# Kernel tuning notes

Measured on AMD Instinct MI355X. Metric: run time of the kernel, lower is better.

The kernel has to match this reference:

```python
import jax, jax.numpy as jnp
import numpy as np

B, T_OUT, C, L = 8, 8, 64, 1024  # batch, temporal channels, spatial channels (=in_channels), time steps


def setup_inputs() -> dict:
    key = jax.random.key(0)
    ks = jax.random.split(key, 7)
    s = 1.0 / np.sqrt(C)  # conv1d default init scale
    return {
        "x": jax.random.normal(ks[0], (B, T_OUT, C, L), dtype=jnp.float32),
        "Wq": jax.random.uniform(ks[1], (C, C), jnp.float32, -s, s),
        "bq": jax.random.uniform(ks[2], (C,), jnp.float32, -s, s),
        "Wk": jax.random.uniform(ks[3], (C, C), jnp.float32, -s, s),
        "bk": jax.random.uniform(ks[4], (C,), jnp.float32, -s, s),
        "Wv": jax.random.uniform(ks[5], (C, C), jnp.float32, -s, s),
        "bv": jax.random.uniform(ks[6], (C,), jnp.float32, -s, s),
    }


def reference(x, Wq, bq, Wk, bk, Wv, bv):
    b, t, c, l = x.shape
    xr = x.reshape(b * t, c, l)  # [BT, C, L]
    # 1x1 Conv1d == per-timestep linear over channels
    q = jnp.einsum('oc,bcl->bol', Wq, xr) + bq[:, None]
    k = jnp.einsum('oc,bcl->bol', Wk, xr) + bk[:, None]
    v = jnp.einsum('oc,bcl->bol', Wv, xr) + bv[:, None]
    # scores[b, i, j] = sum_c q[b, c, i] * k[b, c, j]  -> [BT, L, L]
    scores = jnp.einsum('bci,bcj->bij', q, k)
    weights = jax.nn.softmax(scores, axis=-1)
    # out[b, i, c] = sum_j weights[b, i, j] * v[b, c, j]
    out = jnp.einsum('bij,bcj->bic', weights, v)
    out = jnp.transpose(out, (0, 2, 1))  # [BT, C, L]
    return out.reshape(b, t, c, l)
```

## Files before the change

### kernel.cpp

```cpp
#include <hip/hip_runtime.h>

#define CC 64
#define LL 1024
#define LOG2E 1.44269504f

typedef unsigned short u16;
typedef unsigned int u32;
typedef __attribute__((ext_vector_type(8))) short short8;
typedef __attribute__((ext_vector_type(4))) float floatx4;

static __device__ __forceinline__ u16 f2b(float f) {
  return (u16)((__float_as_uint(f) + 0x8000u) >> 16);
}
static __device__ __forceinline__ u32 pk2(float a, float b) {
  return ((__float_as_uint(a) + 0x8000u) >> 16) |
         ((__float_as_uint(b) + 0x8000u) & 0xffff0000u);
}
static __device__ __forceinline__ u32 pk2t(float a, float b) {
  return __builtin_amdgcn_perm(__float_as_uint(b), __float_as_uint(a), 0x07060302u);
}
static __device__ __forceinline__ short8 mk8(u32 a, u32 b, u32 c, u32 d) {
  union { u32 u[4]; short8 s; } t;
  t.u[0] = a; t.u[1] = b; t.u[2] = c; t.u[3] = d;
  return t.s;
}

#define LDS_U16 28032

__global__ __launch_bounds__(256) void qkv_kernel(
    const float* __restrict__ x,
    const float* __restrict__ Wq, const float* __restrict__ bq,
    const float* __restrict__ Wk, const float* __restrict__ bk,
    const float* __restrict__ Wv, const float* __restrict__ bv,
    u16* __restrict__ qT, u16* __restrict__ kT, u16* __restrict__ vO)
{
  __shared__ __align__(16) u16 smem_u[LDS_U16];
  u16* const whi_s  = smem_u;
  u16* const xh_s   = smem_u + 13824;
  u16* const tbuf_s = smem_u + 23040;
  float* const b_s  = (float*)(smem_u + 27648);

  const int tid  = threadIdx.x;
  const int wave = tid >> 6;
  const int lane = tid & 63;
  const int l16  = lane & 15;
  const int quad = lane >> 4;

  const int bt = blockIdx.x & 63;
  const int l0 = (blockIdx.x >> 6) << 7;

  const int lx = tid & 63;
  const int cg = (tid >> 6) << 4;
  const float* xp = x + ((size_t)bt * CC + cg) * LL + l0 + lx;

  float v0[16];
  #pragma unroll
  for (int e = 0; e < 16; ++e) v0[e] = xp[(size_t)e * LL];

  #pragma unroll
  for (int rep = 0; rep < 24; ++rep) {
    const int i = (rep * 256 + tid) * 2;
    const int m = i >> 12;
    const int r = (i >> 6) & 63;
    const int c = i & 63;
    const int j = i & 4095;
    const float* W = (m == 0) ? Wq : (m == 1) ? Wk : Wv;
    const float sc = (m == 0) ? LOG2E : 1.0f;
    *(u32*)(whi_s + m * 4608 + r * 72 + c) = pk2(W[j] * sc, W[j + 1] * sc);
  }
  if (tid < 192)
    b_s[tid] = (tid < 64) ? bq[tid] * LOG2E
             : (tid < 128) ? bk[tid - 64] : bv[tid - 128];

  #pragma unroll
  for (int e = 0; e < 16; e += 2)
    *(u32*)(xh_s + lx * 72 + cg + e) = pk2(v0[e], v0[e + 1]);
  __syncthreads();

  float v1[16];
  #pragma unroll
  for (int e = 0; e < 16; ++e) v1[e] = xp[64 + (size_t)e * LL];

  u16* tb = tbuf_s + wave * 1152;

  auto compute = [&](int ch) {
    const int lc0 = l0 + (ch << 6);
    const u16* xr_h = xh_s + ch * 4608 + (wave * 16 + l16) * 72 + quad * 8;
    const short8 xh0 = *(const short8*)(xr_h);
    const short8 xh1 = *(const short8*)(xr_h + 32);

    #pragma unroll
    for (int ot = 0; ot < 12; ++ot) {
      const int m = ot >> 2;
      const int off = m * 4608 + ((ot & 3) * 16 + l16) * 72 + quad * 8;
      const short8 ah0 = *(const short8*)(whi_s + off);
      const short8 ah1 = *(const short8*)(whi_s + off + 32);

      floatx4 acc = (floatx4){0.f, 0.f, 0.f, 0.f};
      acc = __builtin_amdgcn_mfma_f32_16x16x32_bf16(ah0, xh0, acc, 0, 0, 0);
      acc = __builtin_amdgcn_mfma_f32_16x16x32_bf16(ah1, xh1, acc, 0, 0, 0);

      float ov[4];
      #pragma unroll
      for (int r = 0; r < 4; ++r)
        ov[r] = acc[r] + b_s[ot * 16 + quad * 4 + r];

      if (ot < 8) {
        uint2 pv;
        pv.x = pk2(ov[0], ov[1]);
        pv.y = pk2(ov[2], ov[3]);
        *(uint2*)(tb + l16 * 72 + (ot & 3) * 16 + quad * 4) = pv;
        if ((ot & 3) == 3) {
          asm volatile("" ::: "memory");
          u16* gdst = ((ot < 4) ? qT : kT) + ((size_t)(bt * LL + lc0 + wave * 16)) * CC;
          const int rr = lane >> 3;
          const int c8 = (lane & 7) * 8;
          #pragma unroll
          for (int s2 = 0; s2 < 2; ++s2) {
            const int row = s2 * 8 + rr;
            uint4 val = *(const uint4*)(tb + row * 72 + c8);
            *(uint4*)(gdst + row * CC + c8) = val;
          }
          asm volatile("" ::: "memory");
        }
      } else {
        const int ob = (ot - 8) * 16 + quad * 4;
        u16* vdst = vO + ((size_t)(bt * CC + ob)) * LL + lc0 + wave * 16 + l16;
        #pragma unroll
        for (int r = 0; r < 4; ++r)
          vdst[(size_t)r * LL] = f2b(ov[r]);
      }
    }
  };

  compute(0);

  #pragma unroll
  for (int e = 0; e < 16; e += 2)
    *(u32*)(xh_s + 4608 + lx * 72 + cg + e) = pk2(v1[e], v1[e + 1]);
  __syncthreads();

  compute(1);
}

__global__ __launch_bounds__(256) void attn_kernel(
    const u16* __restrict__ qT, const u16* __restrict__ kT,
    const u16* __restrict__ vB, float* __restrict__ out)
{
  __shared__ __align__(16) u16 smem[18432];
  const int tid  = threadIdx.x;
  const int wave = tid >> 6;
  const int lane = tid & 63;
  const int l16  = lane & 15;
  const int quad = lane >> 4;

  const int bt    = blockIdx.x & 63;
  const int chunk = blockIdx.x >> 6;
  const int i0w   = (chunk << 6) + (wave << 4);

  const u16* kbase = kT + (size_t)bt * LL * CC;
  const u16* vbase = vB + (size_t)bt * CC * LL;

  short8 qf[2];
  {
    const u16* qr = qT + (size_t)bt * LL * CC + (size_t)(i0w + l16) * CC + quad * 8;
    qf[0] = *(const short8*)(qr);
    qf[1] = *(const short8*)(qr + 32);
  }

  floatx4 O[4];
  #pragma unroll
  for (int cf = 0; cf < 4; ++cf)
    O[cf] = (floatx4){0.f, 0.f, 0.f, 0.f};
  float lsA = 0.f, lsB = 0.f;

  const int r_st = tid >> 2;
  const int c_st = (tid & 3) << 4;
  const int sr = (r_st & 0x20) | ((r_st & 4) << 2) | ((r_st & 0x18) >> 1) | (r_st & 3);

  {
    uint4 k0 = *(const uint4*)(kbase + (size_t)r_st * CC + c_st);
    uint4 k1 = *(const uint4*)(kbase + (size_t)r_st * CC + c_st + 8);
    uint4 v0 = *(const uint4*)(vbase + (size_t)r_st * LL + c_st);
    uint4 v1 = *(const uint4*)(vbase + (size_t)r_st * LL + c_st + 8);
    *(uint4*)(smem + sr * 72 + c_st)              = k0;
    *(uint4*)(smem + sr * 72 + c_st + 8)          = k1;
    *(uint4*)(smem + 4608 + r_st * 72 + c_st)     = v0;
    *(uint4*)(smem + 4608 + r_st * 72 + c_st + 8) = v1;
  }
  __syncthreads();

  for (int it = 0; it < 16; ++it) {
    u16* ktc = smem + (it & 1) * 9216;
    u16* vtc = ktc + 4608;

    uint4 rk0, rk1, rv0, rv1;
    if (it < 15) {
      const int jb = (it + 1) << 6;
      rk0 = *(const uint4*)(kbase + (size_t)(jb + r_st) * CC + c_st);
      rk1 = *(const uint4*)(kbase + (size_t)(jb + r_st) * CC + c_st + 8);
      rv0 = *(const uint4*)(vbase + (size_t)r_st * LL + jb + c_st);
      rv1 = *(const uint4*)(vbase + (size_t)r_st * LL + jb + c_st + 8);
    }

    floatx4 S[4];
    __builtin_amdgcn_s_setprio(1);
    #pragma unroll
    for (int jt = 0; jt < 4; ++jt) {
      const u16* ka = ktc + (jt * 16 + l16) * 72 + quad * 8;
      const short8 a0 = *(const short8*)(ka);
      const short8 a1 = *(const short8*)(ka + 32);
      floatx4 acc = (floatx4){0.f, 0.f, 0.f, 0.f};
      acc = __builtin_amdgcn_mfma_f32_16x16x32_bf16(a0, qf[0], acc, 0, 0, 0);
      acc = __builtin_amdgcn_mfma_f32_16x16x32_bf16(a1, qf[1], acc, 0, 0, 0);
      S[jt] = acc;
    }
    __builtin_amdgcn_s_setprio(0);

    short8 v0f[4], v1f[4];
    #pragma unroll
    for (int cf = 0; cf < 4; ++cf) {
      const u16* va = vtc + (cf * 16 + l16) * 72 + quad * 8;
      v0f[cf] = *(const short8*)(va);
      v1f[cf] = *(const short8*)(va + 32);
    }

    uint2 pp[4];
    #pragma unroll
    for (int jt = 0; jt < 4; ++jt) {
      const float e0 = __builtin_amdgcn_exp2f(S[jt][0]);
      const float e1 = __builtin_amdgcn_exp2f(S[jt][1]);
      const float e2 = __builtin_amdgcn_exp2f(S[jt][2]);
      const float e3 = __builtin_amdgcn_exp2f(S[jt][3]);
      lsA += e0 + e1;
      lsB += e2 + e3;
      pp[jt].x = pk2t(e0, e1);
      pp[jt].y = pk2t(e2, e3);
    }

    __builtin_amdgcn_s_setprio(1);
    {
      const short8 pa0 = mk8(pp[0].x, pp[0].y, pp[1].x, pp[1].y);
      const short8 pa1 = mk8(pp[2].x, pp[2].y, pp[3].x, pp[3].y);
      #pragma unroll
      for (int cf = 0; cf < 4; ++cf) {
        O[cf] = __builtin_amdgcn_mfma_f32_16x16x32_bf16(pa0, v0f[cf], O[cf], 0, 0, 0);
        O[cf] = __builtin_amdgcn_mfma_f32_16x16x32_bf16(pa1, v1f[cf], O[cf], 0, 0, 0);
      }
    }
    __builtin_amdgcn_s_setprio(0);

    if (it < 15) {
      u16* ktn = smem + ((it + 1) & 1) * 9216;
      *(uint4*)(ktn + sr * 72 + c_st)              = rk0;
      *(uint4*)(ktn + sr * 72 + c_st + 8)          = rk1;
      *(uint4*)(ktn + 4608 + r_st * 72 + c_st)     = rv0;
      *(uint4*)(ktn + 4608 + r_st * 72 + c_st + 8) = rv1;
    }
    __syncthreads();
  }

  float lsum = lsA + lsB;
  lsum += __shfl_xor(lsum, 16, 64);
  lsum += __shfl_xor(lsum, 32, 64);

  __syncthreads();
  float* of = (float*)smem + wave * 1280;
  #pragma unroll
  for (int r = 0; r < 4; ++r) {
    const float rl = __builtin_amdgcn_rcpf(__shfl(lsum, quad * 4 + r, 64));
    #pragma unroll
    for (int cf = 0; cf < 4; ++cf)
      O[cf][r] *= rl;
  }
  asm volatile("" ::: "memory");
  #pragma unroll
  for (int cf = 0; cf < 4; ++cf)
    #pragma unroll
    for (int r = 0; r < 4; ++r)
      of[(cf * 16 + l16) * 20 + quad * 4 + r] = O[cf][r];
  asm volatile("" ::: "memory");
  {
    float* ob = out + ((size_t)bt * CC) * LL + i0w;
    #pragma unroll
    for (int rr = 0; rr < 4; ++rr) {
      const int c = rr * 16 + l16;
      float4 val = *(const float4*)(of + c * 20 + quad * 4);
      *(float4*)(ob + (size_t)c * LL + quad * 4) = val;
    }
  }
  asm volatile("" ::: "memory");
}

extern "C" void kernel_launch(void* const* d_in, const int* in_sizes, int n_in,
                              void* d_out, int out_size, void* d_ws, size_t ws_size,
                              hipStream_t stream) {
  const float* x  = (const float*)d_in[0];
  const float* Wq = (const float*)d_in[1];
  const float* bq = (const float*)d_in[2];
  const float* Wk = (const float*)d_in[3];
  const float* bk = (const float*)d_in[4];
  const float* Wv = (const float*)d_in[5];
  const float* bv = (const float*)d_in[6];
  float* out = (float*)d_out;

  u16* qTp = (u16*)d_ws;
  u16* kTp = qTp + (size_t)64 * LL * CC;
  u16* vp  = kTp + (size_t)64 * LL * CC;

  qkv_kernel<<<512, 256, 0, stream>>>(x, Wq, bq, Wk, bk, Wv, bv, qTp, kTp, vp);
  attn_kernel<<<1024, 256, 0, stream>>>(qTp, kTp, vp, out);
}
```

Measured before the change: 114.6 us.

## Precompute bf16 weights in a prep kernel and shrink QKV blocks

A small w_prep kernel now converts Wq/Wk/Wv to bf16 (Q pre-scaled by log2e) and writes them with the biases to workspace once. The QKV kernel then reads weight fragments straight from global/L2 instead of staging them in LDS, and each block handles 64 time steps instead of 128, doubling the grid to 1024 blocks with less LDS per block. This removes the per-block weight conversion and staging, and raises occupancy. The cost is an extra kernel launch and weight loads from global memory on every MFMA tile. A sched_barrier was also added after the prefetch loads in the attention kernel to pin the instruction order.

After: 122.8 us. +7.1%, slower.

```diff
diff --git a/kernel.cpp b/kernel.cpp
--- a/kernel.cpp
+++ b/kernel.cpp
@@ -25,20 +25,30 @@
   return t.s;
 }
 
-#define LDS_U16 28032
-
-__global__ __launch_bounds__(256) void qkv_kernel(
-    const float* __restrict__ x,
+__global__ __launch_bounds__(256) void w_prep(
     const float* __restrict__ Wq, const float* __restrict__ bq,
     const float* __restrict__ Wk, const float* __restrict__ bk,
     const float* __restrict__ Wv, const float* __restrict__ bv,
+    u16* __restrict__ whi, float* __restrict__ bsc)
+{
+  const int idx = blockIdx.x * 256 + threadIdx.x;
+  const int m = idx >> 12;
+  const float* W = (m == 0) ? Wq : (m == 1) ? Wk : Wv;
+  const float w = W[idx & 4095] * ((m == 0) ? LOG2E : 1.0f);
+  whi[idx] = f2b(w);
+  if (blockIdx.x == 0 && threadIdx.x < 192)
+    bsc[threadIdx.x] = (threadIdx.x < 64) ? bq[threadIdx.x] * LOG2E
+                     : (threadIdx.x < 128) ? bk[threadIdx.x - 64] : bv[threadIdx.x - 128];
+}
+
+__global__ __launch_bounds__(256) void qkv_kernel(
+    const float* __restrict__ x,
+    const u16* __restrict__ whi, const float* __restrict__ bsc,
     u16* __restrict__ qT, u16* __restrict__ kT, u16* __restrict__ vO)
 {
-  __shared__ __align__(16) u16 smem_u[LDS_U16];
-  u16* const whi_s  = smem_u;
-  u16* const xh_s   = smem_u + 13824;
-  u16* const tbuf_s = smem_u + 23040;
-  float* const b_s  = (float*)(smem_u + 27648);
+  __shared__ __align__(16) u16 xh_s[64 * 72];
+  __shared__ __align__(16) u16 tbuf_s[4 * 16 * 72];
+  __shared__ float b_s[192];
 
   const int tid  = threadIdx.x;
   const int wave = tid >> 6;
@@ -47,7 +57,7 @@
   const int quad = lane >> 4;
 
   const int bt = blockIdx.x & 63;
-  const int l0 = (blockIdx.x >> 6) << 7;
+  const int l0 = (blockIdx.x >> 6) << 6;
 
   const int lx = tid & 63;
   const int cg = (tid >> 6) << 4;
@@ -56,91 +66,60 @@
   float v0[16];
   #pragma unroll
   for (int e = 0; e < 16; ++e) v0[e] = xp[(size_t)e * LL];
-
-  #pragma unroll
-  for (int rep = 0; rep < 24; ++rep) {
-    const int i = (rep * 256 + tid) * 2;
-    const int m = i >> 12;
-    const int r = (i >> 6) & 63;
-    const int c = i & 63;
-    const int j = i & 4095;
-    const float* W = (m == 0) ? Wq : (m == 1) ? Wk : Wv;
-    const float sc = (m == 0) ? LOG2E : 1.0f;
-    *(u32*)(whi_s + m * 4608 + r * 72 + c) = pk2(W[j] * sc, W[j + 1] * sc);
-  }
-  if (tid < 192)
-    b_s[tid] = (tid < 64) ? bq[tid] * LOG2E
-             : (tid < 128) ? bk[tid - 64] : bv[tid - 128];
-
+  if (tid < 192) b_s[tid] = bsc[tid];
   #pragma unroll
   for (int e = 0; e < 16; e += 2)
     *(u32*)(xh_s + lx * 72 + cg + e) = pk2(v0[e], v0[e + 1]);
   __syncthreads();
 
-  float v1[16];
-  #pragma unroll
-  for (int e = 0; e < 16; ++e) v1[e] = xp[64 + (size_t)e * LL];
+  const u16* xr_h = xh_s + (wave * 16 + l16) * 72 + quad * 8;
+  const short8 xh0 = *(const short8*)(xr_h);
+  const short8 xh1 = *(const short8*)(xr_h + 32);
 
   u16* tb = tbuf_s + wave * 1152;
 
-  auto compute = [&](int ch) {
-    const int lc0 = l0 + (ch << 6);
-    const u16* xr_h = xh_s + ch * 4608 + (wave * 16 + l16) * 72 + quad * 8;
-    const short8 xh0 = *(const short8*)(xr_h);
-    const short8 xh1 = *(const short8*)(xr_h + 32);
-
-    #pragma unroll
-    for (int ot = 0; ot < 12; ++ot) {
-      const int m = ot >> 2;
-      const int off = m * 4608 + ((ot & 3) * 16 + l16) * 72 + quad * 8;
-      const short8 ah0 = *(const short8*)(whi_s + off);
-      const short8 ah1 = *(const short8*)(whi_s + off + 32);
-
-      floatx4 acc = (floatx4){0.f, 0.f, 0.f, 0.f};
-      acc = __builtin_amdgcn_mfma_f32_16x16x32_bf16(ah0, xh0, acc, 0, 0, 0);
-      acc = __builtin_amdgcn_mfma_f32_16x16x32_bf16(ah1, xh1, acc, 0, 0, 0);
-
-      float ov[4];
+  #pragma unroll
+  for (int ot = 0; ot < 12; ++ot) {
+    const int m = ot >> 2;
+    const int off = (m << 12) + (((ot & 3) * 16 + l16) << 6) + quad * 8;
+    const short8 ah0 = *(const short8*)(whi + off);
+    const short8 ah1 = *(const short8*)(whi + off + 32);
+
+    floatx4 acc = (floatx4){0.f, 0.f, 0.f, 0.f};
+    acc = __builtin_amdgcn_mfma_f32_16x16x32_bf16(ah0, xh0, acc, 0, 0, 0);
+    acc = __builtin_amdgcn_mfma_f32_16x16x32_bf16(ah1, xh1, acc, 0, 0, 0);
+
+    float ov[4];
+    #pragma unroll
+    for (int r = 0; r < 4; ++r)
+      ov[r] = acc[r] + b_s[ot * 16 + quad * 4 + r];
+
+    if (ot < 8) {
+      uint2 pv;
+      pv.x = pk2(ov[0], ov[1]);
+      pv.y = pk2(ov[2], ov[3]);
+      *(uint2*)(tb + l16 * 72 + (ot & 3) * 16 + quad * 4) = pv;
+      if ((ot & 3) == 3) {
+        asm volatile("" ::: "memory");
+        u16* gdst = ((ot < 4) ? qT : kT) + ((size_t)(bt * LL + l0 + wave * 16)) * CC;
+        const int rr = lane >> 3;
+        const int c8 = (lane & 7) * 8;
+        #pragma unroll
+        for (int s2 = 0; s2 < 2; ++s2) {
+          const int row = s2 * 8 + rr;
+          uint4 val = *(const uint4*)(tb + row * 72 + c8);
+          *(uint4*)(gdst + row * CC + c8) = val;
+        }
+        asm volatile("" ::: "memory");
+      }
+    } else {
+      const int ob = (ot - 8) * 16 + quad * 4;
+      u16* vdst = vO + ((size_t)(bt * CC + ob)) * LL + l0 + wave * 16 + l16;
       #pragma unroll
       for (int r = 0; r < 4; ++r)
-        ov[r] = acc[r] + b_s[ot * 16 + quad * 4 + r];
-
-      if (ot < 8) {
-        uint2 pv;
-        pv.x = pk2(ov[0], ov[1]);
-        pv.y = pk2(ov[2], ov[3]);
-        *(uint2*)(tb + l16 * 72 + (ot & 3) * 16 + quad * 4) = pv;
-        if ((ot & 3) == 3) {
-          asm volatile("" ::: "memory");
-          u16* gdst = ((ot < 4) ? qT : kT) + ((size_t)(bt * LL + lc0 + wave * 16)) * CC;
-          const int rr = lane >> 3;
-          const int c8 = (lane & 7) * 8;
-          #pragma unroll
-          for (int s2 = 0; s2 < 2; ++s2) {
-            const int row = s2 * 8 + rr;
-            uint4 val = *(const uint4*)(tb + row * 72 + c8);
-            *(uint4*)(gdst + row * CC + c8) = val;
-          }
-          asm volatile("" ::: "memory");
-        }
-      } else {
-        const int ob = (ot - 8) * 16 + quad * 4;
-        u16* vdst = vO + ((size_t)(bt * CC + ob)) * LL + lc0 + wave * 16 + l16;
-        #pragma unroll
-        for (int r = 0; r < 4; ++r)
-          vdst[(size_t)r * LL] = f2b(ov[r]);
-      }
-    }
-  };
-
-  compute(0);
-
-  #pragma unroll
-  for (int e = 0; e < 16; e += 2)
-    *(u32*)(xh_s + 4608 + lx * 72 + cg + e) = pk2(v1[e], v1[e + 1]);
-  __syncthreads();
-
-  compute(1);
+        vdst[(size_t)r * LL] = f2b(ov[r]);
+    }
+  }
 }
 
 __global__ __launch_bounds__(256) void attn_kernel(
@@ -201,6 +180,7 @@
       rk1 = *(const uint4*)(kbase + (size_t)(jb + r_st) * CC + c_st + 8);
       rv0 = *(const uint4*)(vbase + (size_t)r_st * LL + jb + c_st);
       rv1 = *(const uint4*)(vbase + (size_t)r_st * LL + jb + c_st + 8);
+      __builtin_amdgcn_sched_barrier(0);
     }
 
     floatx4 S[4];
@@ -307,7 +287,10 @@
   u16* qTp = (u16*)d_ws;
   u16* kTp = qTp + (size_t)64 * LL * CC;
   u16* vp  = kTp + (size_t)64 * LL * CC;
-
-  qkv_kernel<<<512, 256, 0, stream>>>(x, Wq, bq, Wk, bk, Wv, bv, qTp, kTp, vp);
+  u16* whi = vp  + (size_t)64 * LL * CC;
+  float* bsc = (float*)(whi + 3 * 64 * 64);
+
+  w_prep<<<48, 256, 0, stream>>>(Wq, bq, Wk, bk, Wv, bv, whi, bsc);
+  qkv_kernel<<<1024, 256, 0, stream>>>(x, whi, bsc, qTp, kTp, vp);
   attn_kernel<<<1024, 256, 0, stream>>>(qTp, kTp, vp, out);
 }
```
